# Kernel tuning notes

Hardware: AMD Instinct MI355X
Metric: run time of the kernel (lower is better)

Reference implementation:

```python
import jax, jax.numpy as jnp
import numpy as np

N = 131072
D = 1024
L = 128
B = 64  # number of bags / segments
TEMP = 1.0
EPS = 1e-12  # F.normalize eps


def setup_inputs() -> dict:
    key = jax.random.key(0)
    ks = jax.random.split(key, 5)
    feature = jax.random.normal(ks[0], (N, D), dtype=jnp.float32)
    batch = jnp.sort(jax.random.randint(ks[1], (N,), 0, B)).astype(jnp.int64)
    # xavier_normal_ std = sqrt(2 / (fan_in + fan_out))
    Wa = jax.random.normal(ks[2], (L, D), dtype=jnp.float32) * np.sqrt(2.0 / (D + L))
    Wb = jax.random.normal(ks[3], (L, D), dtype=jnp.float32) * np.sqrt(2.0 / (D + L))
    Wc = jax.random.normal(ks[4], (1, L), dtype=jnp.float32) * np.sqrt(2.0 / (L + 1))
    ba = jnp.zeros((L,), dtype=jnp.float32)
    bb = jnp.zeros((L,), dtype=jnp.float32)
    bc = jnp.zeros((1,), dtype=jnp.float32)
    return {"feature": feature, "batch": batch, "Wa": Wa, "ba": ba,
            "Wb": Wb, "bb": bb, "Wc": Wc, "bc": bc}


def reference(feature, batch, Wa, ba, Wb, bb, Wc, bc):
    # F.normalize: L2-normalize each row
    norm = jnp.linalg.norm(feature, axis=1, keepdims=True)
    feature = feature / jnp.maximum(norm, EPS)

    # gated attention score
    a = jax.nn.sigmoid(feature @ Wa.T + ba)            # [N, L]
    b = jnp.tanh(feature @ Wb.T + bb)                  # [N, L]
    score = ((a * b) @ Wc.T + bc) / TEMP               # [N, 1]

    # segment softmax over bags (torch_geometric softmax(score, batch))
    s = score[:, 0]                                    # [N]
    seg_max = jax.ops.segment_max(s, batch, num_segments=B)
    e = jnp.exp(s - seg_max[batch])
    denom = jax.ops.segment_sum(e, batch, num_segments=B)
    score = (e / denom[batch])[:, None]                # [N, 1]

    # scatter-sum pooling (dropout omitted: eval-mode determinism)
    out = jax.ops.segment_sum(score * feature, batch, num_segments=B)  # [B, D]
    return (out, score, feature)
```

## Files before the change

kernel.cpp:

```cpp
#include <hip/hip_runtime.h>
#include <cstdint>
#include <cstddef>

#define NROWS 131072
#define DDIM  1024
#define LDIM  128
#define BSEG  64
#define FIX2  281474976710656.0

typedef float f32x4 __attribute__((ext_vector_type(4)));
typedef short short8 __attribute__((ext_vector_type(8)));

__device__ inline unsigned short f2bf(float f) {
    union { float f; unsigned u; } x; x.f = f;
    unsigned u = x.u + 0x7fffu + ((x.u >> 16) & 1u);
    return (unsigned short)(u >> 16);
}

__device__ inline int lower_bound_dev(const int* __restrict__ arr, int n, int v) {
    int lo = 0, hi = n;
    while (lo < hi) { int mid = (lo + hi) >> 1; if (arr[mid] < v) lo = mid + 1; else hi = mid; }
    return lo;
}

__global__ void wconv_kernel(const float* __restrict__ Wa, const float* __restrict__ Wb,
                             unsigned short* __restrict__ wpre) {
    int n  = blockIdx.x;
    int kt = threadIdx.x >> 4;
    int q  = threadIdx.x & 15;
    const float* wrow = (n < LDIM) ? (Wa + (size_t)n * DDIM)
                                   : (Wb + (size_t)(n - LDIM) * DDIM);
    float4 v = *(const float4*)(wrow + kt * 64 + q * 4);
    ushort4 h;
    h.x = f2bf(v.x); h.y = f2bf(v.y); h.z = f2bf(v.z); h.w = f2bf(v.w);
    int w, nfi, rA;
    if (n < LDIM) { w = n >> 4; nfi = 0; rA = n & 15; }
    else { int m = n - LDIM; w = m >> 4; nfi = 1; rA = m & 15; }
    int kk    = q >> 3;
    int e     = (q & 7) * 4;
    int kl    = e >> 3;
    int inner = (e & 7) * 2;
    int lane  = kl * 16 + rA;
    int f     = ((kt * 2 + kk) * 8 + w) * 2 + nfi;
    *(ushort4*)((char*)wpre + f * 1024 + lane * 16 + inner) = h;
}

__global__ __launch_bounds__(512, 6)
void gemm_kernel(const float* __restrict__ feat, const unsigned short* __restrict__ wpre,
                 const float* __restrict__ ba, const float* __restrict__ bb,
                 const float* __restrict__ Wc, const float* __restrict__ bc,
                 const int* __restrict__ batch,
                 float* __restrict__ nf_out, float* __restrict__ s_out,
                 unsigned long long* __restrict__ acc64)
{
    __shared__ __align__(16) char smem[35584];
    float* invA_l = (float*)(smem + 32768);
    float* part   = (float*)(smem + 33024);
    float* u_row  = (float*)(smem + 35072);
    int*   seg_l  = (int*)(smem + 35328);

    const int tid  = threadIdx.x;
    const int w    = tid >> 6;
    const int lane = tid & 63;
    const int rblk = blockIdx.x * 64;
    const int sr   = tid >> 3;
    const int sc8  = tid & 7;

    if (tid < 64) seg_l[tid] = batch[rblk + tid];

    const float4* rowp4 = (const float4*)(feat + (size_t)(rblk + sr) * DDIM);

    f32x4 acc[4][2];
    #pragma unroll
    for (int i = 0; i < 4; ++i)
        #pragma unroll
        for (int j = 0; j < 2; ++j)
            acc[i][j] = (f32x4){0.f, 0.f, 0.f, 0.f};

    const int rA  = lane & 15;
    const int kl  = lane >> 4;
    const int swz = (lane & 7) << 4;
    const char* wsrc = (const char*)wpre + w * 2048 + lane * 16;

    float sq = 0.f;

    #pragma unroll
    for (int j = 0; j < 2; ++j) {
        int cf = sc8 + j * 8;
        float4 v = rowp4[cf];
        sq += v.x * v.x + v.y * v.y + v.z * v.z + v.w * v.w;
        ushort4 h;
        h.x = f2bf(v.x); h.y = f2bf(v.y); h.z = f2bf(v.z); h.w = f2bf(v.w);
        *(ushort4*)(smem + ((sr * 128 + cf * 8) ^ ((sr & 7) << 4))) = h;
    }
    __syncthreads();

    int cur = 0;
    for (int kt = 0; kt < 16; ++kt) {
        float4 av[2];
        if (kt < 15) {
            #pragma unroll
            for (int j = 0; j < 2; ++j)
                av[j] = rowp4[(kt + 1) * 16 + sc8 + j * 8];
        }
        short8 wf[4];
        #pragma unroll
        for (int q = 0; q < 4; ++q)
            wf[q] = *(const short8*)(wsrc + (size_t)kt * 32768 + (q >> 1) * 16384 + (q & 1) * 1024);
        {
            const char* Abuf = smem + cur * 16384;
            #pragma unroll
            for (int kk = 0; kk < 2; ++kk) {
                int koff = (kk * 64 + kl * 16) ^ swz;
                #pragma unroll
                for (int mf = 0; mf < 4; ++mf) {
                    short8 af = *(const short8*)(Abuf + (mf * 16 + rA) * 128 + koff);
                    #pragma unroll
                    for (int nfi = 0; nfi < 2; ++nfi)
                        acc[mf][nfi] = __builtin_amdgcn_mfma_f32_16x16x32_bf16(
                            af, wf[kk * 2 + nfi], acc[mf][nfi], 0, 0, 0);
                }
            }
        }
        if (kt < 15) {
            char* Abuf = smem + (cur ^ 1) * 16384;
            #pragma unroll
            for (int j = 0; j < 2; ++j) {
                int cf = sc8 + j * 8;
                float4 v = av[j];
                sq += v.x * v.x + v.y * v.y + v.z * v.z + v.w * v.w;
                ushort4 h;
                h.x = f2bf(v.x); h.y = f2bf(v.y); h.z = f2bf(v.z); h.w = f2bf(v.w);
                *(ushort4*)(Abuf + ((sr * 128 + cf * 8) ^ ((sr & 7) << 4))) = h;
            }
        }
        __syncthreads();
        cur ^= 1;
    }

    sq += __shfl_xor(sq, 1, 64);
    sq += __shfl_xor(sq, 2, 64);
    sq += __shfl_xor(sq, 4, 64);
    if (sc8 == 0) invA_l[sr] = 1.f / fmaxf(sqrtf(sq), 1e-12f);
    __syncthreads();

    {
        int l0 = w * 16 + rA;
        float ba0 = ba[l0], bb0 = bb[l0], wc0 = Wc[l0];
        float vals[4][4];
        #pragma unroll
        for (int mf = 0; mf < 4; ++mf)
            #pragma unroll
            for (int reg = 0; reg < 4; ++reg) {
                int r = mf * 16 + kl * 4 + reg;
                float ia = invA_l[r];
                float pa0 = acc[mf][0][reg] * ia + ba0;
                float pb0 = acc[mf][1][reg] * ia + bb0;
                float a0 = 1.f / (1.f + __expf(-pa0));
                float b0 = 1.f - 2.f / (1.f + __expf(2.f * pb0));
                vals[mf][reg] = a0 * b0 * wc0;
            }
        #pragma unroll
        for (int mf = 0; mf < 4; ++mf)
            #pragma unroll
            for (int reg = 0; reg < 4; ++reg) {
                float v = vals[mf][reg];
                v += __shfl_xor(v, 1, 64);
                v += __shfl_xor(v, 2, 64);
                v += __shfl_xor(v, 4, 64);
                v += __shfl_xor(v, 8, 64);
                vals[mf][reg] = v;
            }
        if (rA == 0) {
            #pragma unroll
            for (int mf = 0; mf < 4; ++mf)
                #pragma unroll
                for (int reg = 0; reg < 4; ++reg)
                    part[w * 64 + mf * 16 + kl * 4 + reg] = vals[mf][reg];
        }
    }
    __syncthreads();
    if (tid < 64) {
        float s = part[tid] + part[64 + tid] + part[128 + tid] + part[192 + tid]
                + part[256 + tid] + part[320 + tid] + part[384 + tid] + part[448 + tid] + bc[0];
        u_row[tid] = __expf(s);
        s_out[rblk + tid] = s;
    }
    __syncthreads();

    {
        const int col = tid & 255;
        const int grp = tid >> 8;
        const float4* __restrict__ fbase = (const float4*)(feat + (size_t)rblk * DDIM);
        float4*       __restrict__ nbase = (float4*)(nf_out + (size_t)rblk * DDIM);
        float ax = 0.f, ay = 0.f, az = 0.f, aw = 0.f;
        int curseg = seg_l[grp];
        for (int rr = 0; rr < 8; ++rr) {
            int r0 = rr * 8 + grp;
            float4 v0 = fbase[(r0 + 0) * 256 + col];
            float4 v1 = fbase[(r0 + 2) * 256 + col];
            float4 v2 = fbase[(r0 + 4) * 256 + col];
            float4 v3 = fbase[(r0 + 6) * 256 + col];
            #pragma unroll
            for (int j = 0; j < 4; ++j) {
                int r = r0 + j * 2;
                float4 v = (j == 0) ? v0 : (j == 1) ? v1 : (j == 2) ? v2 : v3;
                int sg = seg_l[r];
                if (sg != curseg) {
                    unsigned long long* dst = acc64 + (size_t)curseg * DDIM + col * 4;
                    atomicAdd(&dst[0], (unsigned long long)(long long)((double)ax * FIX2));
                    atomicAdd(&dst[1], (unsigned long long)(long long)((double)ay * FIX2));
                    atomicAdd(&dst[2], (unsigned long long)(long long)((double)az * FIX2));
                    atomicAdd(&dst[3], (unsigned long long)(long long)((double)aw * FIX2));
                    ax = ay = az = aw = 0.f;
                    curseg = sg;
                }
                float ia = invA_l[r];
                float u  = u_row[r];
                v.x *= ia; v.y *= ia; v.z *= ia; v.w *= ia;
                nbase[r * 256 + col] = v;
                ax += u * v.x; ay += u * v.y; az += u * v.z; aw += u * v.w;
            }
        }
        unsigned long long* dst = acc64 + (size_t)curseg * DDIM + col * 4;
        atomicAdd(&dst[0], (unsigned long long)(long long)((double)ax * FIX2));
        atomicAdd(&dst[1], (unsigned long long)(long long)((double)ay * FIX2));
        atomicAdd(&dst[2], (unsigned long long)(long long)((double)az * FIX2));
        atomicAdd(&dst[3], (unsigned long long)(long long)((double)aw * FIX2));
    }
}

__global__ void softmax_kernel(const int* __restrict__ batch, float* __restrict__ score,
                               float* __restrict__ smax, float* __restrict__ ssum) {
    int b = blockIdx.x;
    int tid = threadIdx.x;
    int start = lower_bound_dev(batch, NROWS, b);
    int end   = lower_bound_dev(batch, NROWS, b + 1);
    __shared__ float red[4];
    __shared__ float bm, bd;

    float m = -INFINITY;
    for (int i = start + tid; i < end; i += 256) m = fmaxf(m, score[i]);
    #pragma unroll
    for (int k = 1; k < 64; k <<= 1) m = fmaxf(m, __shfl_xor(m, k, 64));
    if ((tid & 63) == 0) red[tid >> 6] = m;
    __syncthreads();
    if (tid == 0) bm = fmaxf(fmaxf(red[0], red[1]), fmaxf(red[2], red[3]));
    __syncthreads();
    float M = bm;

    float sum = 0.f;
    for (int i = start + tid; i < end; i += 256) sum += __expf(score[i] - M);
    #pragma unroll
    for (int k = 1; k < 64; k <<= 1) sum += __shfl_xor(sum, k, 64);
    if ((tid & 63) == 0) red[tid >> 6] = sum;
    __syncthreads();
    if (tid == 0) { bd = red[0] + red[1] + red[2] + red[3]; smax[b] = bm; ssum[b] = bd; }
    __syncthreads();
    float invD = 1.f / bd;

    for (int i = start + tid; i < end; i += 256)
        score[i] = __expf(score[i] - M) * invD;
}

__global__ void finalize_kernel(const unsigned long long* __restrict__ acc64,
                                const float* __restrict__ smax, const float* __restrict__ ssum,
                                float* __restrict__ out) {
    int i = blockIdx.x * 256 + threadIdx.x;
    int b = i >> 10;
    double denom = exp((double)smax[b]) * (double)ssum[b];
    out[i] = (float)(((double)(long long)acc64[i]) * (1.0 / FIX2) / denom);
}

extern "C" void kernel_launch(void* const* d_in, const int* in_sizes, int n_in,
                              void* d_out, int out_size, void* d_ws, size_t ws_size,
                              hipStream_t stream) {
    const float* feat  = (const float*)d_in[0];
    const int*   batch = (const int*)d_in[1];
    const float* Wa = (const float*)d_in[2];
    const float* ba = (const float*)d_in[3];
    const float* Wb = (const float*)d_in[4];
    const float* bb = (const float*)d_in[5];
    const float* Wc = (const float*)d_in[6];
    const float* bc = (const float*)d_in[7];

    float* out_seg = (float*)d_out;
    float* score   = out_seg + (size_t)BSEG * DDIM;
    float* nf      = score + NROWS;

    unsigned short*     wpre  = (unsigned short*)d_ws;
    unsigned long long* acc64 = (unsigned long long*)((char*)d_ws + 524288);
    float* smax = (float*)d_ws;
    float* ssum = smax + BSEG;

    hipMemsetAsync(acc64, 0, (size_t)BSEG * DDIM * 8, stream);
    wconv_kernel<<<256, 256, 0, stream>>>(Wa, Wb, wpre);
    gemm_kernel<<<NROWS / 64, 512, 0, stream>>>(feat, wpre, ba, bb, Wc, bc, batch,
                                                nf, score, acc64);
    softmax_kernel<<<BSEG, 256, 0, stream>>>(batch, score, smax, ssum);
    finalize_kernel<<<BSEG * DDIM / 256, 256, 0, stream>>>(acc64, smax, ssum, out_seg);
}
```

Before: 383.7 us.

## Stream fp32 feature tiles directly to LDS and convert to bf16 at fragment load

Replaces the register-staged global-load, bf16-convert and LDS-store path with global_load_lds direct-to-LDS copies of fp32 tiles in a swizzled layout. The bf16 conversion and the row sum-of-squares now happen when each wave reads its MFMA fragments from LDS, and the norm reduction is reworked to match. This removes VGPR staging and the store pass, but doubles LDS bytes per tile and repeats the conversion in every wave that reads the same fragments. The buffers are sized 16KB per stage for 64 rows x 64 fp32, which appears to match the existing smem layout.

```diff
diff --git a/kernel.cpp b/kernel.cpp
--- a/kernel.cpp
+++ b/kernel.cpp
@@ -1,4 +1,5 @@
 #include <hip/hip_runtime.h>
+#include <hip/hip_bf16.h>
 #include <cstdint>
 #include <cstddef>
 
@@ -21,6 +22,12 @@
     int lo = 0, hi = n;
     while (lo < hi) { int mid = (lo + hi) >> 1; if (arr[mid] < v) lo = mid + 1; else hi = mid; }
     return lo;
+}
+
+__device__ inline void gload_lds16(const void* g, void* l) {
+    __builtin_amdgcn_global_load_lds(
+        (const __attribute__((address_space(1))) unsigned int*)g,
+        (__attribute__((address_space(3))) unsigned int*)l, 16, 0, 0);
 }
 
 __global__ void wconv_kernel(const float* __restrict__ Wa, const float* __restrict__ Wb,
@@ -63,12 +70,17 @@
     const int w    = tid >> 6;
     const int lane = tid & 63;
     const int rblk = blockIdx.x * 64;
-    const int sr   = tid >> 3;
-    const int sc8  = tid & 7;
+    const int rA   = lane & 15;
+    const int kl   = lane >> 4;
 
     if (tid < 64) seg_l[tid] = batch[rblk + tid];
 
-    const float4* rowp4 = (const float4*)(feat + (size_t)(rblk + sr) * DDIM);
+    const int srow0 = w * 8 + (lane >> 4);
+    const int srow1 = srow0 + 4;
+    const float* s0 = feat + (size_t)(rblk + srow0) * DDIM
+                    + (((((lane & 15) * 16) ^ ((srow0 & 15) << 4))) >> 2);
+    const float* s1 = feat + (size_t)(rblk + srow1) * DDIM
+                    + (((((lane & 15) * 16) ^ ((srow1 & 15) << 4))) >> 2);
 
     f32x4 acc[4][2];
     #pragma unroll
@@ -77,71 +89,56 @@
         for (int j = 0; j < 2; ++j)
             acc[i][j] = (f32x4){0.f, 0.f, 0.f, 0.f};
 
-    const int rA  = lane & 15;
-    const int kl  = lane >> 4;
-    const int swz = (lane & 7) << 4;
     const char* wsrc = (const char*)wpre + w * 2048 + lane * 16;
-
     float sq = 0.f;
 
-    #pragma unroll
-    for (int j = 0; j < 2; ++j) {
-        int cf = sc8 + j * 8;
-        float4 v = rowp4[cf];
-        sq += v.x * v.x + v.y * v.y + v.z * v.z + v.w * v.w;
-        ushort4 h;
-        h.x = f2bf(v.x); h.y = f2bf(v.y); h.z = f2bf(v.z); h.w = f2bf(v.w);
-        *(ushort4*)(smem + ((sr * 128 + cf * 8) ^ ((sr & 7) << 4))) = h;
-    }
+    gload_lds16(s0, smem + w * 2048);
+    gload_lds16(s1, smem + w * 2048 + 1024);
     __syncthreads();
 
     int cur = 0;
     for (int kt = 0; kt < 16; ++kt) {
-        float4 av[2];
-        if (kt < 15) {
-            #pragma unroll
-            for (int j = 0; j < 2; ++j)
-                av[j] = rowp4[(kt + 1) * 16 + sc8 + j * 8];
-        }
         short8 wf[4];
         #pragma unroll
         for (int q = 0; q < 4; ++q)
             wf[q] = *(const short8*)(wsrc + (size_t)kt * 32768 + (q >> 1) * 16384 + (q & 1) * 1024);
+        if (kt < 15) {
+            char* dst = smem + (cur ^ 1) * 16384 + w * 2048;
+            gload_lds16(s0 + (kt + 1) * 64, dst);
+            gload_lds16(s1 + (kt + 1) * 64, dst + 1024);
+        }
         {
-            const char* Abuf = smem + cur * 16384;
+            const char* Ab = smem + cur * 16384;
             #pragma unroll
             for (int kk = 0; kk < 2; ++kk) {
-                int koff = (kk * 64 + kl * 16) ^ swz;
                 #pragma unroll
                 for (int mf = 0; mf < 4; ++mf) {
-                    short8 af = *(const short8*)(Abuf + (mf * 16 + rA) * 128 + koff);
+                    const int row = mf * 16 + rA;
+                    const int g   = kk * 128 + kl * 32;
+                    f32x4 lo = *(const f32x4*)(Ab + row * 256 + (g ^ (rA << 4)));
+                    f32x4 hi = *(const f32x4*)(Ab + row * 256 + ((g + 16) ^ (rA << 4)));
+                    if (mf == w)
+                        sq += lo[0]*lo[0] + lo[1]*lo[1] + lo[2]*lo[2] + lo[3]*lo[3]
+                            + hi[0]*hi[0] + hi[1]*hi[1] + hi[2]*hi[2] + hi[3]*hi[3];
+                    union { short8 s; __hip_bfloat162 b2[4]; } r;
+                    r.b2[0] = __float22bfloat162_rn(make_float2(lo[0], lo[1]));
+                    r.b2[1] = __float22bfloat162_rn(make_float2(lo[2], lo[3]));
+                    r.b2[2] = __float22bfloat162_rn(make_float2(hi[0], hi[1]));
+                    r.b2[3] = __float22bfloat162_rn(make_float2(hi[2], hi[3]));
                     #pragma unroll
                     for (int nfi = 0; nfi < 2; ++nfi)
                         acc[mf][nfi] = __builtin_amdgcn_mfma_f32_16x16x32_bf16(
-                            af, wf[kk * 2 + nfi], acc[mf][nfi], 0, 0, 0);
+                            r.s, wf[kk * 2 + nfi], acc[mf][nfi], 0, 0, 0);
                 }
-            }
-        }
-        if (kt < 15) {
-            char* Abuf = smem + (cur ^ 1) * 16384;
-            #pragma unroll
-            for (int j = 0; j < 2; ++j) {
-                int cf = sc8 + j * 8;
-                float4 v = av[j];
-                sq += v.x * v.x + v.y * v.y + v.z * v.z + v.w * v.w;
-                ushort4 h;
-                h.x = f2bf(v.x); h.y = f2bf(v.y); h.z = f2bf(v.z); h.w = f2bf(v.w);
-                *(ushort4*)(Abuf + ((sr * 128 + cf * 8) ^ ((sr & 7) << 4))) = h;
             }
         }
         __syncthreads();
         cur ^= 1;
     }
 
-    sq += __shfl_xor(sq, 1, 64);
-    sq += __shfl_xor(sq, 2, 64);
-    sq += __shfl_xor(sq, 4, 64);
-    if (sc8 == 0) invA_l[sr] = 1.f / fmaxf(sqrtf(sq), 1e-12f);
+    sq += __shfl_xor(sq, 16, 64);
+    sq += __shfl_xor(sq, 32, 64);
+    if (w < 4 && lane < 16) invA_l[w * 16 + rA] = 1.f / fmaxf(sqrtf(sq), 1e-12f);
     __syncthreads();
 
     {
```

After: 360.7 us. -6.0%, faster.
